# Performance work log

Measured on AMD Instinct MI355X. Metric: run time of the kernel, lower is better.

The kernel has to match this reference:

```python
import jax, jax.numpy as jnp
import numpy as np

B, N_IN, D_IN, N_OUT, D_OUT = 16, 256, 128, 128, 64
W_INIT_CONST = float(np.sqrt(N_OUT / (D_IN * N_IN)))


def setup_inputs() -> dict:
    key = jax.random.key(0)
    k1, k2, k3 = jax.random.split(key, 3)
    x = jax.random.normal(k1, (B, N_IN, D_IN), dtype=jnp.float32)
    current_act = jax.random.uniform(k2, (B, N_IN), dtype=jnp.float32)
    W = W_INIT_CONST * jax.random.normal(k3, (N_IN, D_IN, N_OUT, D_OUT), dtype=jnp.float32)
    return {"input": x, "current_act": current_act, "W": W, "num_iter": 1}


def reference(input, current_act, W, num_iter):
    scale = 1.0 / np.sqrt(D_OUT)
    # votes[b,n,m,d] = sum_a input[b,n,a] * W[n,a,m,d]  -- the big bilinear product,
    # computed once and reused for score computation and the final weighted reduce.
    votes = jnp.einsum('bna,namd->bnmd', input, W)  # [B, N_IN, N_OUT, D_OUT]

    # next_capsule_value is None -> uniform query_key = softmax(zeros) = 1/N_OUT
    ncv = votes.sum(axis=1) / N_OUT  # [B, N_OUT, D_OUT]

    # next_act is None -> mean activation broadcast to all output capsules
    next_act = jnp.broadcast_to(current_act.mean(axis=1, keepdims=True), (B, N_OUT))

    # attention-like routing coefficients
    scores = jnp.einsum('bnmd,bmd->bnm', votes, ncv) * scale  # [B, N_IN, N_OUT]
    qk = jax.nn.softmax(scores, axis=2) * next_act[:, None, :]
    qk = qk / (qk.sum(axis=2, keepdims=True) + 1e-10)

    # weighted reduce of votes, gated by input activations
    next_capsule_value = jnp.einsum('bnm,bn,bnmd->bmd', qk, current_act, votes)
    return (next_capsule_value, next_act, qk)
```

## Files before the change

### kernel.cpp

```cpp
#include <hip/hip_runtime.h>
#include <hip/hip_bf16.h>
#include <cstdint>


#define BB 16
#define N_IN 256
#define D_IN 128
#define N_OUT 128
#define D_OUT 64
#define MD (N_OUT * D_OUT)
#define NPB 2
#define NCH 32

__global__ __launch_bounds__(256) void pass0_xT(
    const float* __restrict__ x, float* __restrict__ xT)
{
    const int idx = blockIdx.x * 256 + threadIdx.x;
    const int b = idx & 15;
    const int a = (idx >> 4) & 127;
    const int n = idx >> 11;
    xT[idx] = x[((size_t)b * N_IN + n) * D_IN + a];
}

__global__ __launch_bounds__(256, 4) void pass1_votes(
    const float* __restrict__ xT, const float* __restrict__ W,
    uint2* __restrict__ votes4)
{
    __shared__ float xs[NPB * D_IN * BB];
    const int t = threadIdx.x;
    const int chunk = blockIdx.x;
    const int ng = blockIdx.y;
    const int j = chunk * 1024 + t * 4;

    {
        const float4* src = reinterpret_cast<const float4*>(xT + ((size_t)ng * NPB << 11));
        float4* dst = reinterpret_cast<float4*>(xs);
#pragma unroll
        for (int r = 0; r < 4; ++r) dst[r * 256 + t] = src[r * 256 + t];
    }
    __syncthreads();

    for (int ni = 0; ni < NPB; ++ni) {
        const int n = ng * NPB + ni;
        const float4* __restrict__ Wp =
            reinterpret_cast<const float4*>(W + (size_t)n * D_IN * MD + j);

        float acc[BB][4];
#pragma unroll
        for (int b = 0; b < BB; ++b) {
            acc[b][0] = 0.f; acc[b][1] = 0.f; acc[b][2] = 0.f; acc[b][3] = 0.f;
        }

#pragma unroll 4
        for (int a = 0; a < D_IN; ++a) {
            const float4 w = Wp[(size_t)a * (MD / 4)];
            const float4* xa = reinterpret_cast<const float4*>(xs + (ni * D_IN + a) * BB);
            const float4 x0 = xa[0], x1 = xa[1], x2 = xa[2], x3 = xa[3];
            const float xv[BB] = {x0.x, x0.y, x0.z, x0.w, x1.x, x1.y, x1.z, x1.w,
                                  x2.x, x2.y, x2.z, x2.w, x3.x, x3.y, x3.z, x3.w};
#pragma unroll
            for (int b = 0; b < BB; ++b) {
                acc[b][0] = fmaf(xv[b], w.x, acc[b][0]);
                acc[b][1] = fmaf(xv[b], w.y, acc[b][1]);
                acc[b][2] = fmaf(xv[b], w.z, acc[b][2]);
                acc[b][3] = fmaf(xv[b], w.w, acc[b][3]);
            }
        }

#pragma unroll
        for (int b = 0; b < BB; ++b) {
            union { __hip_bfloat16 h[4]; uint2 u; } pk;
            pk.h[0] = __float2bfloat16(acc[b][0]);
            pk.h[1] = __float2bfloat16(acc[b][1]);
            pk.h[2] = __float2bfloat16(acc[b][2]);
            pk.h[3] = __float2bfloat16(acc[b][3]);
            votes4[(((size_t)b * N_IN + n) * MD + j) >> 2] = pk.u;
        }
    }
}

__global__ __launch_bounds__(256) void pass_ncv_part(
    const uint32_t* __restrict__ votes2, float* __restrict__ ncv_part)
{
    const int t = threadIdx.x;
    const int jc = blockIdx.x;
    const int nh = blockIdx.y;
    const int b  = blockIdx.z;
    const int j = jc * 1024 + t * 4;

    const uint2* vp = reinterpret_cast<const uint2*>(votes2) +
                      ((((size_t)b * N_IN + (size_t)nh * 64) * MD + j) >> 2);
    float s0 = 0.f, s1 = 0.f, s2 = 0.f, s3 = 0.f;
#pragma unroll 8
    for (int n = 0; n < 64; ++n) {
        const uint2 u = vp[(size_t)n * (MD / 4)];
        s0 += __uint_as_float(u.x << 16);
        s1 += __uint_as_float(u.x & 0xffff0000u);
        s2 += __uint_as_float(u.y << 16);
        s3 += __uint_as_float(u.y & 0xffff0000u);
    }
    float4 o; o.x = s0; o.y = s1; o.z = s2; o.w = s3;
    *reinterpret_cast<float4*>(ncv_part + ((size_t)nh * BB + b) * MD + j) = o;
}

__global__ __launch_bounds__(256) void pass3_route(
    const __hip_bfloat16* __restrict__ votes, const float* __restrict__ ncv_part,
    const float* __restrict__ act, float* __restrict__ out_part,
    float* __restrict__ next_act_out, float* __restrict__ qk_out)
{
    __shared__ float red[4];
    __shared__ float aw[4];
    const int t = threadIdx.x;
    const int b = blockIdx.x;
    const int nc = blockIdx.y;
    const int m = t >> 1;
    const int half = t & 1;

    float av = act[b * N_IN + t];
#pragma unroll
    for (int off = 32; off; off >>= 1) av += __shfl_xor(av, off);
    if ((t & 63) == 0) aw[t >> 6] = av;
    __syncthreads();
    const float amean = (aw[0] + aw[1] + aw[2] + aw[3]) * (1.f / 256.f);
    const float qs = amean / (amean + 1e-10f);
    if (nc == 0 && half == 0) next_act_out[b * N_OUT + m] = amean;

    float nv[32], oacc[32];
    {
        const float4* p0 = reinterpret_cast<const float4*>(ncv_part + ((size_t)0 * BB + b) * MD + t * 32);
        const float4* p1 = reinterpret_cast<const float4*>(ncv_part + ((size_t)1 * BB + b) * MD + t * 32);
        const float4* p2 = reinterpret_cast<const float4*>(ncv_part + ((size_t)2 * BB + b) * MD + t * 32);
        const float4* p3 = reinterpret_cast<const float4*>(ncv_part + ((size_t)3 * BB + b) * MD + t * 32);
#pragma unroll
        for (int q = 0; q < 8; ++q) {
            const float4 a0 = p0[q], a1 = p1[q], a2 = p2[q], a3 = p3[q];
            nv[4 * q + 0] = (a0.x + a1.x) + (a2.x + a3.x);
            nv[4 * q + 1] = (a0.y + a1.y) + (a2.y + a3.y);
            nv[4 * q + 2] = (a0.z + a1.z) + (a2.z + a3.z);
            nv[4 * q + 3] = (a0.w + a1.w) + (a2.w + a3.w);
        }
#pragma unroll
        for (int i = 0; i < 32; ++i) { nv[i] *= (1.f / (float)N_OUT); oacc[i] = 0.f; }
    }

    const uint4* vbase = reinterpret_cast<const uint4*>(
        votes + (size_t)b * ((size_t)N_IN * MD) + (size_t)(nc * 8) * MD + t * 32);
    const size_t nstride = MD / 8;

    uint4 buf[4];
#pragma unroll
    for (int q = 0; q < 4; ++q) buf[q] = vbase[q];

    for (int ni = 0; ni < 8; ++ni) {
        const int n = nc * 8 + ni;
        float vv[32];
#pragma unroll
        for (int q = 0; q < 4; ++q) {
            const uint32_t ww[4] = {buf[q].x, buf[q].y, buf[q].z, buf[q].w};
#pragma unroll
            for (int k = 0; k < 4; ++k) {
                vv[8 * q + 2 * k]     = __uint_as_float(ww[k] << 16);
                vv[8 * q + 2 * k + 1] = __uint_as_float(ww[k] & 0xffff0000u);
            }
        }
        if (ni < 7) {
            const uint4* vn = vbase + (size_t)(ni + 1) * nstride;
#pragma unroll
            for (int q = 0; q < 4; ++q) buf[q] = vn[q];
        }

        float p0 = 0.f, p1 = 0.f, p2 = 0.f, p3 = 0.f;
#pragma unroll
        for (int i = 0; i < 8; ++i) {
            p0 = fmaf(vv[4 * i + 0], nv[4 * i + 0], p0);
            p1 = fmaf(vv[4 * i + 1], nv[4 * i + 1], p1);
            p2 = fmaf(vv[4 * i + 2], nv[4 * i + 2], p2);
            p3 = fmaf(vv[4 * i + 3], nv[4 * i + 3], p3);
        }
        float sp = (p0 + p1) + (p2 + p3);
        sp += __shfl_xor(sp, 1);
        sp *= 0.125f;

        const float p = __expf(sp);
        float s = p;
#pragma unroll
        for (int off = 32; off; off >>= 1) s += __shfl_xor(s, off);
        if ((t & 63) == 0) red[t >> 6] = s;
        __syncthreads();
        const float ssum = (red[0] + red[1] + red[2] + red[3]) * 0.5f;
        __syncthreads();

        const float qk = (p / ssum) * qs;
        if (half == 0) qk_out[((size_t)(b * N_IN + n) << 7) + m] = qk;

        const float c = qk * act[b * N_IN + n];
#pragma unroll
        for (int i = 0; i < 32; ++i) oacc[i] = fmaf(c, vv[i], oacc[i]);
    }

    float4* op = reinterpret_cast<float4*>(out_part + ((size_t)nc * BB + b) * MD + t * 32);
#pragma unroll
    for (int q = 0; q < 8; ++q) {
        float4 o; o.x = oacc[4 * q]; o.y = oacc[4 * q + 1];
        o.z = oacc[4 * q + 2]; o.w = oacc[4 * q + 3];
        op[q] = o;
    }
}

__global__ __launch_bounds__(256) void combine_out0(
    const float* __restrict__ out_part, float* __restrict__ out0)
{
    const int idx = blockIdx.x * 256 + threadIdx.x;
    const int b = idx >> 11;
    const int v4 = idx & 2047;
    const float4* p = reinterpret_cast<const float4*>(out_part);
    float4 s = {0.f, 0.f, 0.f, 0.f};
#pragma unroll 8
    for (int nc = 0; nc < NCH; ++nc) {
        const float4 f = p[((size_t)nc * BB + b) * (MD / 4) + v4];
        s.x += f.x; s.y += f.y; s.z += f.z; s.w += f.w;
    }
    reinterpret_cast<float4*>(out0)[idx] = s;
}

extern "C" void kernel_launch(void* const* d_in, const int* in_sizes, int n_in,
                              void* d_out, int out_size, void* d_ws, size_t ws_size,
                              hipStream_t stream)
{
    const float* x   = (const float*)d_in[0];
    const float* act = (const float*)d_in[1];
    const float* W   = (const float*)d_in[2];

    float* out      = (float*)d_out;
    float* out0     = out;
    float* next_act = out + 131072;
    float* qk_out   = out + 131072 + 2048;

    __hip_bfloat16* votes = (__hip_bfloat16*)d_ws;
    float* ncv_part = (float*)((char*)d_ws + (size_t)67108864);
    float* out_part = (float*)((char*)d_ws + (size_t)67108864 + 2097152);
    float* xT       = (float*)((char*)d_ws + (size_t)67108864 + 2097152 + 16777216);

    pass0_xT<<<2048, 256, 0, stream>>>(x, xT);
    pass1_votes<<<dim3(8, 128), 256, 0, stream>>>(xT, W, (uint2*)votes);
    pass_ncv_part<<<dim3(8, 4, 16), 256, 0, stream>>>((const uint32_t*)votes, ncv_part);
    pass3_route<<<dim3(16, NCH), 256, 0, stream>>>(votes, ncv_part, act, out_part,
                                                   next_act, qk_out);
    combine_out0<<<128, 256, 0, stream>>>(out_part, out0);
}
```

Measured before the change: 272.0 us.

## Double-buffer W tiles into LDS via async global_load_lds in votes kernel

The votes GEMM kernel now streams W through a two-stage LDS ring buffer using direct global-to-LDS loads, with explicit vmcnt waits and barriers, instead of each thread loading float4s straight from global memory. The goal is to overlap W fetches with FMA work and hide memory latency. It adds 32KB of shared memory per block and drops the occupancy hint from the launch bounds, which may lower occupancy. It also adds per-tile barriers and fragile manual wait counts.

```diff
diff --git a/kernel.cpp b/kernel.cpp
--- a/kernel.cpp
+++ b/kernel.cpp
@@ -11,6 +11,16 @@
 #define MD (N_OUT * D_OUT)
 #define NPB 2
 #define NCH 32
+#define TA 4
+#define NT (D_IN / TA)
+
+__device__ __forceinline__ void gload16(const float* g, float* l) {
+    __builtin_amdgcn_global_load_lds(
+        (const __attribute__((address_space(1))) void*)g,
+        (__attribute__((address_space(3))) void*)l, 16, 0, 0);
+}
+#define VM4 asm volatile("s_waitcnt vmcnt(4)" ::: "memory")
+#define VM0 asm volatile("s_waitcnt vmcnt(0)" ::: "memory")
 
 __global__ __launch_bounds__(256) void pass0_xT(
     const float* __restrict__ x, float* __restrict__ xT)
@@ -22,15 +32,18 @@
     xT[idx] = x[((size_t)b * N_IN + n) * D_IN + a];
 }
 
-__global__ __launch_bounds__(256, 4) void pass1_votes(
+__global__ __launch_bounds__(256) void pass1_votes(
     const float* __restrict__ xT, const float* __restrict__ W,
     uint2* __restrict__ votes4)
 {
     __shared__ float xs[NPB * D_IN * BB];
+    __shared__ float wb[2][TA * 1024];
     const int t = threadIdx.x;
+    const int wid = t >> 6, lane = t & 63;
     const int chunk = blockIdx.x;
     const int ng = blockIdx.y;
-    const int j = chunk * 1024 + t * 4;
+    const int jbase = chunk * 1024;
+    const int j = jbase + t * 4;
 
     {
         const float4* src = reinterpret_cast<const float4*>(xT + ((size_t)ng * NPB << 11));
@@ -42,8 +55,7 @@
 
     for (int ni = 0; ni < NPB; ++ni) {
         const int n = ng * NPB + ni;
-        const float4* __restrict__ Wp =
-            reinterpret_cast<const float4*>(W + (size_t)n * D_IN * MD + j);
+        const float* Wn = W + (size_t)n * D_IN * MD + jbase;
 
         float acc[BB][4];
 #pragma unroll
@@ -51,19 +63,51 @@
             acc[b][0] = 0.f; acc[b][1] = 0.f; acc[b][2] = 0.f; acc[b][3] = 0.f;
         }
 
-#pragma unroll 4
-        for (int a = 0; a < D_IN; ++a) {
-            const float4 w = Wp[(size_t)a * (MD / 4)];
-            const float4* xa = reinterpret_cast<const float4*>(xs + (ni * D_IN + a) * BB);
-            const float4 x0 = xa[0], x1 = xa[1], x2 = xa[2], x3 = xa[3];
-            const float xv[BB] = {x0.x, x0.y, x0.z, x0.w, x1.x, x1.y, x1.z, x1.w,
-                                  x2.x, x2.y, x2.z, x2.w, x3.x, x3.y, x3.z, x3.w};
-#pragma unroll
-            for (int b = 0; b < BB; ++b) {
-                acc[b][0] = fmaf(xv[b], w.x, acc[b][0]);
-                acc[b][1] = fmaf(xv[b], w.y, acc[b][1]);
-                acc[b][2] = fmaf(xv[b], w.z, acc[b][2]);
-                acc[b][3] = fmaf(xv[b], w.w, acc[b][3]);
+        auto stage = [&](int tk, int pb) {
+#pragma unroll
+            for (int q = 0; q < 4; ++q) {
+                const float* g = Wn + (size_t)(tk * TA + wid) * MD + q * 256 + lane * 4;
+                float* l = &wb[pb][wid * 1024 + q * 256];
+                gload16(g, l);
+            }
+        };
+        auto compute = [&](int tk, int pb) {
+#pragma unroll
+            for (int al = 0; al < TA; ++al) {
+                const int a = tk * TA + al;
+                const float4 w = *reinterpret_cast<const float4*>(&wb[pb][al * 1024 + t * 4]);
+                const float4* xa = reinterpret_cast<const float4*>(xs + (ni * D_IN + a) * BB);
+                const float4 x0 = xa[0], x1 = xa[1], x2 = xa[2], x3 = xa[3];
+                const float xv[BB] = {x0.x, x0.y, x0.z, x0.w, x1.x, x1.y, x1.z, x1.w,
+                                      x2.x, x2.y, x2.z, x2.w, x3.x, x3.y, x3.z, x3.w};
+#pragma unroll
+                for (int b = 0; b < BB; ++b) {
+                    acc[b][0] = fmaf(xv[b], w.x, acc[b][0]);
+                    acc[b][1] = fmaf(xv[b], w.y, acc[b][1]);
+                    acc[b][2] = fmaf(xv[b], w.z, acc[b][2]);
+                    acc[b][3] = fmaf(xv[b], w.w, acc[b][3]);
+                }
+            }
+        };
+
+        stage(0, 0);
+        stage(1, 1);
+        VM4;
+        __builtin_amdgcn_sched_barrier(0);
+        __builtin_amdgcn_s_barrier();
+
+        for (int tk = 0; tk < NT; ++tk) {
+            compute(tk, tk & 1);
+            __builtin_amdgcn_s_barrier();
+            if (tk < NT - 2) {
+                stage(tk + 2, tk & 1);
+                VM4;
+            } else if (tk == NT - 2) {
+                VM0;
+            }
+            if (tk < NT - 1) {
+                __builtin_amdgcn_sched_barrier(0);
+                __builtin_amdgcn_s_barrier();
             }
         }
 
@@ -76,6 +120,7 @@
             pk.h[3] = __float2bfloat16(acc[b][3]);
             votes4[(((size_t)b * N_IN + n) * MD + j) >> 2] = pk.u;
         }
+        if (ni == 0) __builtin_amdgcn_s_barrier();
     }
 }
 
```

Result: slower. 282.7 us (+3.9%).
